# Kernel tuning notes

Hardware: AMD Instinct MI355X
Metric: run time of the kernel (lower is better)

## Reference

```python
import jax, jax.numpy as jnp
import numpy as np

G, N, E = 16, 512, 2048        # graphs, nodes/graph, edges/graph
CN, CE = 64, 64                # node / edge feature channels
K = 3                          # Laguerre polynomial order
RATIO = 0.5
KEEP = int(np.ceil(RATIO * N)) # 256 kept nodes per graph (static)
POWER_ITERS = 64               # power iteration approximating eigsh(k=1,'LM')


def setup_inputs() -> dict:
    key = jax.random.key(0)
    ks = jax.random.split(key, 10)
    x_n = jax.random.normal(ks[0], (G * N, CN), jnp.float32)
    x_e = jax.random.normal(ks[1], (G * E, CE), jnp.float32)
    # incidence endpoints per edge, local node ids, no self loops
    u = jax.random.randint(ks[2], (G, E), 0, N)
    v = (u + 1 + jax.random.randint(ks[3], (G, E), 0, N - 1)) % N
    # node-level conv graph (global ids within per-graph blocks): both directions
    offs = (jnp.arange(G) * N)[:, None]
    src_n = jnp.concatenate([(u + offs).reshape(-1), (v + offs).reshape(-1)])
    dst_n = jnp.concatenate([(v + offs).reshape(-1), (u + offs).reshape(-1)])
    edge_weight_n = jax.random.uniform(ks[4], (src_n.shape[0],), jnp.float32)
    # edge-level conv graph (global ids within per-graph edge blocks)
    ME = 4 * E
    offs_e = (jnp.arange(G) * E)[:, None]
    src_e = (jax.random.randint(ks[5], (G, ME), 0, E) + offs_e).reshape(-1)
    dst_e = (jax.random.randint(ks[6], (G, ME), 0, E) + offs_e).reshape(-1)
    edge_weight_e = jax.random.uniform(ks[7], (src_e.shape[0],), jnp.float32)
    # HodgeLaguerreConv(C -> 1, K) weights (glorot-ish) + bias (zeros init)
    W_n = jax.random.normal(ks[8], (K, CN), jnp.float32) / np.sqrt(CN)
    b_n = jnp.zeros((1,), jnp.float32)
    W_e = jax.random.normal(ks[9], (K, CE), jnp.float32) / np.sqrt(CE)
    b_e = jnp.zeros((1,), jnp.float32)
    return dict(x_n=x_n, x_e=x_e, edge_u=u, edge_v=v,
                src_n=src_n, dst_n=dst_n, edge_weight_n=edge_weight_n,
                src_e=src_e, dst_e=dst_e, edge_weight_e=edge_weight_e,
                W_n=W_n, b_n=b_n, W_e=W_e, b_e=b_e)


def hodge_laguerre(x, src, dst, w, Wk, b):
    """HodgeLaguerreConv with out_channels=1: out = sum_k T_k(L) x @ Wk[k] + b.
    T_0 = x; T_1 = x - Lx; T_{k+1} = (-L T_k + (2k+1) T_k - k T_{k-1})/(k+1)."""
    num = x.shape[0]
    def L(z):  # scatter-add message passing: out[i] = sum_{j->i} norm * z[j]
        return jax.ops.segment_sum(w[:, None] * z[src], dst, num_segments=num)
    Tx0 = x
    out = Tx0 @ Wk[0]
    Tx1 = x - L(x)
    out = out + Tx1 @ Wk[1]
    k = 1
    for i in range(2, Wk.shape[0]):
        Tx2 = (-L(Tx1) + (2 * k + 1) * Tx1 - k * Tx0) / (k + 1)
        out = out + Tx2 @ Wk[i]
        Tx0, Tx1 = Tx1, Tx2
        k += 1
    return out + b[0]


def pool_graph(sn, se, xn, xe, u, v):
    # node score augmented by |B1| @ edge_score (abs incidence gathers both endpoints)
    aug = sn.at[u].add(se).at[v].add(se)
    perm = jnp.argsort(-aug)                    # descending sort, take top KEEP
    mask_n = jnp.zeros((N,), xn.dtype).at[perm[:KEEP]].set(1.0)
    # mask_e = |B1|^T (1 - mask_n); keep edge iff both endpoints kept (== 0)
    bad = (1.0 - mask_n[u]) + (1.0 - mask_n[v])
    keep_e = (bad == 0.0).astype(xn.dtype)
    # dense incidence B1 [N, E]: -1 at source row, +1 at target row
    cols = jnp.arange(E)
    B = jnp.zeros((N, E), xn.dtype).at[u, cols].add(-1.0).at[v, cols].add(1.0)
    Bm = B * mask_n[:, None] * keep_e[None, :]  # row/col masking (zero-padded)
    L0 = Bm @ Bm.T                              # [N, N] node Laplacian
    L1 = Bm.T @ Bm                              # [E, E] edge Laplacian
    # power iteration for lambda_max(L0) (== eigsh k=1 'LM'; zero rows keep spectrum)
    w = jnp.ones((N,), xn.dtype) / np.sqrt(N)
    for _ in range(POWER_ITERS):
        w = L0 @ w
        w = w / (jnp.linalg.norm(w) + 1e-12)
    lam = w @ (L0 @ w)
    scale = 2.0 / (lam + 1e-12)
    return xn * mask_n[:, None], L0 * scale, xe * keep_e[:, None], L1 * scale


def reference(x_n, x_e, edge_u, edge_v, src_n, dst_n, edge_weight_n,
              src_e, dst_e, edge_weight_e, W_n, b_n, W_e, b_e):
    score_n = jax.nn.sigmoid(hodge_laguerre(x_n, src_n, dst_n, edge_weight_n, W_n, b_n).reshape(-1))
    score_e = jax.nn.sigmoid(hodge_laguerre(x_e, src_e, dst_e, edge_weight_e, W_e, b_e).reshape(-1))
    xn_g = (x_n * score_n[:, None]).reshape(G, N, CN)
    xe_g = (x_e * score_e[:, None]).reshape(G, E, CE)
    sn = score_n.reshape(G, N)
    se = score_e.reshape(G, E)
    return jax.vmap(pool_graph)(sn, se, xn_g, xe_g, edge_u, edge_v)
```

## Files before the change

kernel.cpp:

```cpp
#include <hip/hip_runtime.h>
#include <math.h>

#define GG 16
#define NNODE 512
#define EEDGE 2048
#define KEEPN 256
#define PITERS 64
#define NNT 8192
#define NET 32768

typedef float vfloat4 __attribute__((ext_vector_type(4)));

#define WS_C1N 0
#define WS_C2N 8192
#define WS_BN  16384
#define WS_C1E 24576
#define WS_C2E 57344
#define WS_BE  90112
#define WS_SNW 122880
#define WS_SEW 131072
#define WS_KLIST 163840
#define WS_KCNT 196608
#define WS_SCALE 196624

#define O_XN 0
#define O_L0 524288
#define O_XE 4718592
#define O_L1 6815744

#define L04 1048576
#define ZTOT4 17825792
#define ZA4 6291456

__global__ __launch_bounds__(256) void k_dots(const float* __restrict__ xn,
    const float* __restrict__ xe, const float* __restrict__ Wn,
    const float* __restrict__ We, float* __restrict__ ws, float* __restrict__ out) {
  if (blockIdx.x >= 10240) {
    vfloat4 z = (vfloat4)(0.f);
    vfloat4* o4 = (vfloat4*)out;
    int start = (blockIdx.x - 10240) * 256 + threadIdx.x;
    #pragma unroll
    for (int n = 0; n < 24; ++n) {
      int i = start + n * 262144;
      int f = (i < L04) ? (O_L0 / 4 + i) : (O_L1 / 4 + (i - L04));
      __builtin_nontemporal_store(z, &o4[f]);
    }
    return;
  }
  int gw = (blockIdx.x * 256 + threadIdx.x) >> 6;
  int lane = threadIdx.x & 63;
  const float* x; const float* W; int row; float *c1, *c2, *bs;
  if (gw < NNT) {
    row = gw; x = xn + (size_t)row * 64; W = Wn;
    c1 = ws + WS_C1N; c2 = ws + WS_C2N; bs = ws + WS_BN;
  } else {
    row = gw - NNT;
    x = xe + (size_t)row * 64; W = We;
    c1 = ws + WS_C1E; c2 = ws + WS_C2E; bs = ws + WS_BE;
  }
  float v = x[lane];
  float r0 = v * W[lane];
  float r1 = v * W[64 + lane];
  float r2 = v * W[128 + lane];
  for (int o = 32; o; o >>= 1) {
    r0 += __shfl_xor(r0, o, 64);
    r1 += __shfl_xor(r1, o, 64);
    r2 += __shfl_xor(r2, o, 64);
  }
  if (lane == 0) { c1[row] = r1; c2[row] = r2; bs[row] = r0 + r1 + r2; }
}

#define SM_AUG 0
#define SM_SNW 512
#define SM_RED 1024
#define SM_IWS 1032
#define SM_KCP 1040
#define SM_S0  1056
#define SM_TOT 9256
#define DCAP 12
__global__ __launch_bounds__(512) void k_pool(
    const int* __restrict__ src_n, const int* __restrict__ dst_n, const float* __restrict__ wn,
    const int* __restrict__ src_e, const int* __restrict__ dst_e, const float* __restrict__ we,
    const int* __restrict__ edge_u, const int* __restrict__ edge_v,
    const float* __restrict__ bnp, const float* __restrict__ bep,
    float* __restrict__ ws, float* __restrict__ out) {
  const int tid = threadIdx.x;
  if (blockIdx.x >= 16) {
    vfloat4 z = (vfloat4)(0.f);
    vfloat4* o4 = (vfloat4*)out;
    int start = ZA4 + (blockIdx.x - 16) * 512 + tid;
    #pragma unroll
    for (int n = 0; n < 11; ++n) {
      int i = start + n * 1048576;
      __builtin_nontemporal_store(z, &o4[O_L1 / 4 + (i - L04)]);
    }
    return;
  }
  __shared__ float smem[SM_TOT];
  int* smi = (int*)smem;
  float* aug = smem + SM_AUG;
  float* snw = smem + SM_SNW;
  float* red = smem + SM_RED;
  int*   iws = smi + SM_IWS;
  int*   kcp = smi + SM_KCP;

  const int g = blockIdx.x;
  const int roffN = g * NNODE;
  const int roffE = g * EEDGE;
  const int lane = tid & 63, wid = tid >> 6;
  float biasN = bnp[0], biasE = bep[0];

  {
    float* c1n = smem + SM_S0;
    float* c2n = smem + SM_S0 + 512;
    float* d1n = smem + SM_S0 + 1024;
    float* d2n = smem + SM_S0 + 1536;
    float* e2n = smem + SM_S0 + 2048;
    c1n[tid] = ws[WS_C1N + roffN + tid];
    c2n[tid] = ws[WS_C2N + roffN + tid];
    d1n[tid] = 0.f; d2n[tid] = 0.f; e2n[tid] = 0.f;
    __syncthreads();
    for (int t = tid; t < 4096; t += 512) {
      int idx = (t < 2048) ? (g * 2048 + t) : (32768 + g * 2048 + (t - 2048));
      int s = src_n[idx] - roffN, d = dst_n[idx] - roffN;
      float w = wn[idx];
      atomicAdd(&d1n[d], w * c1n[s]);
      atomicAdd(&d2n[d], w * c2n[s]);
    }
    __syncthreads();
    for (int t = tid; t < 4096; t += 512) {
      int idx = (t < 2048) ? (g * 2048 + t) : (32768 + g * 2048 + (t - 2048));
      int s = src_n[idx] - roffN, d = dst_n[idx] - roffN;
      atomicAdd(&e2n[d], wn[idx] * d2n[s]);
    }
    __syncthreads();
    float t = ws[WS_BN + roffN + tid] - d1n[tid] - 2.0f * d2n[tid]
            + 0.5f * e2n[tid] + biasN;
    float s = 1.0f / (1.0f + expf(-t));
    snw[tid] = s; aug[tid] = s;
    __syncthreads();
  }

  float* seS = smem + SM_S0 + 2048;
  int*   suv = smi + SM_S0;
  {
    float* c1e = smem + SM_S0;
    float* c2e = smem + SM_S0 + 2048;
    float* d1e = smem + SM_S0 + 4096;
    float* d2e = smem + SM_S0 + 6144;
    float* e2e = smem + SM_S0;
    for (int i = tid; i < EEDGE; i += 512) {
      c1e[i] = ws[WS_C1E + roffE + i];
      c2e[i] = ws[WS_C2E + roffE + i];
      d1e[i] = 0.f; d2e[i] = 0.f;
    }
    __syncthreads();
    for (int t = tid; t < 8192; t += 512) {
      int idx = g * 8192 + t;
      int s = src_e[idx] - roffE, d = dst_e[idx] - roffE;
      float w = we[idx];
      atomicAdd(&d1e[d], w * c1e[s]);
      atomicAdd(&d2e[d], w * c2e[s]);
    }
    __syncthreads();
    for (int i = tid; i < EEDGE; i += 512) e2e[i] = 0.f;
    __syncthreads();
    for (int t = tid; t < 8192; t += 512) {
      int idx = g * 8192 + t;
      int s = src_e[idx] - roffE, d = dst_e[idx] - roffE;
      atomicAdd(&e2e[d], we[idx] * d2e[s]);
    }
    __syncthreads();
    for (int e = tid; e < EEDGE; e += 512) {
      float t = ws[WS_BE + roffE + e] - d1e[e] - 2.0f * d2e[e]
              + 0.5f * e2e[e] + biasE;
      float s = 1.0f / (1.0f + expf(-t));
      int u = edge_u[roffE + e], v = edge_v[roffE + e];
      seS[e] = s;
      suv[e] = u | (v << 16);
      atomicAdd(&aug[u], s);
      atomicAdd(&aug[v], s);
    }
    __syncthreads();
  }

  unsigned short* adjU = (unsigned short*)(smem + SM_S0 + 4096);
  float* wvA = smem + SM_S0 + 6144;
  float* wvB = smem + SM_S0 + 6660;
  int* maskS = smi + SM_S0 + 7176;
  int* degS  = smi + SM_S0 + 7688;
  int* offS  = smi + SM_SNW;

  {
    float a = aug[tid];
    int r = 0;
    #pragma unroll 8
    for (int j = 0; j < NNODE; ++j) {
      float b = aug[j];
      r += (b > a) || (b == a && j < tid);
    }
    maskS[tid] = (r < KEEPN) ? 1 : 0;
    degS[tid] = 0;
  }
  if (tid == 0) *kcp = 0;
  __syncthreads();
  ws[WS_SNW + roffN + tid] = snw[tid] * (float)maskS[tid];

  int* wsi = (int*)ws;
  for (int e = tid; e < EEDGE; e += 512) {
    int p2 = suv[e];
    int u = p2 & 0xffff, v = p2 >> 16;
    int k = maskS[u] & maskS[v];
    ws[WS_SEW + roffE + e] = seS[e] * (float)k;
    if (k) {
      int p = atomicAdd(kcp, 1);
      wsi[WS_KLIST + roffE + p] = e;
      atomicAdd(&degS[u], 1);
      atomicAdd(&degS[v], 1);
    }
  }
  __syncthreads();
  if (tid == 0) wsi[WS_KCNT + g] = *kcp;

  int dv = degS[tid];
  int inc = dv;
  for (int o = 1; o < 64; o <<= 1) {
    int t = __shfl_up(inc, o, 64);
    if (lane >= o) inc += t;
  }
  if (lane == 63) iws[wid] = inc;
  __syncthreads();
  int base = 0;
  for (int k = 0; k < wid; ++k) base += iws[k];
  int myStart = base + inc - dv;
  offS[tid] = myStart;
  __syncthreads();

  for (int e = tid; e < EEDGE; e += 512) {
    int p2 = suv[e];
    int u = p2 & 0xffff, v = p2 >> 16;
    if (maskS[u] & maskS[v]) {
      int pu = atomicAdd(&offS[u], 1); adjU[pu] = (unsigned short)v;
      int pv = atomicAdd(&offS[v], 1); adjU[pv] = (unsigned short)u;
    }
  }
  __syncthreads();
  int myDeg = dv;
  int myEnd = myStart + myDeg;

  int nbr[DCAP];
  #pragma unroll
  for (int k = 0; k < DCAP; ++k)
    nbr[k] = (k < myDeg) ? (int)adjU[myStart + k] : NNODE;
  bool ovf = myDeg > DCAP;

  wvA[tid] = 0.04419417382415922f;
  if (tid == 0) { wvA[NNODE] = 0.f; wvB[NNODE] = 0.f; }
  __syncthreads();
  float* wcur = wvA; float* wnext = wvB;
  for (int it = 0; it < PITERS; ++it) {
    float acc = (float)myDeg * wcur[tid];
    #pragma unroll
    for (int k = 0; k < DCAP; ++k) acc -= wcur[nbr[k]];
    if (ovf) for (int p = myStart + DCAP; p < myEnd; ++p) acc -= wcur[(int)adjU[p]];
    if ((it & 7) == 7) {
      float sq = acc * acc;
      for (int o = 32; o; o >>= 1) sq += __shfl_xor(sq, o, 64);
      if (lane == 0) red[wid] = sq;
      __syncthreads();
      float tot = red[0] + red[1] + red[2] + red[3]
                + red[4] + red[5] + red[6] + red[7];
      wnext[tid] = acc * (1.0f / (sqrtf(tot) + 1e-12f));
    } else {
      wnext[tid] = acc;
    }
    __syncthreads();
    float* tmp = wcur; wcur = wnext; wnext = tmp;
  }
  {
    float wv_ = wcur[tid];
    float acc = (float)myDeg * wv_;
    #pragma unroll
    for (int k = 0; k < DCAP; ++k) acc -= wcur[nbr[k]];
    if (ovf) for (int p = myStart + DCAP; p < myEnd; ++p) acc -= wcur[(int)adjU[p]];
    float pr = wv_ * acc;
    for (int o = 32; o; o >>= 1) pr += __shfl_xor(pr, o, 64);
    if (lane == 0) red[wid] = pr;
    __syncthreads();
    if (tid == 0) {
      float lam = red[0] + red[1] + red[2] + red[3]
                + red[4] + red[5] + red[6] + red[7];
      ws[WS_SCALE + g] = 2.0f / (lam + 1e-12f);
    }
  }
}

__global__ __launch_bounds__(256) void k_out(
    const float* __restrict__ xn, const float* __restrict__ xe,
    const int* __restrict__ edge_u, const int* __restrict__ edge_v,
    const float* __restrict__ ws, float* __restrict__ out) {
  int b = blockIdx.x, tid = threadIdx.x;
  const int* wsi = (const int*)ws;
  if (b < 512) {
    int idx = b * 256 + tid;
    int row = idx >> 4;
    float s = ws[WS_SNW + row];
    float4 x4 = ((const float4*)xn)[idx];
    ((float4*)(out + O_XN))[idx] = make_float4(x4.x * s, x4.y * s, x4.z * s, x4.w * s);
  } else if (b < 2560) {
    int idx = (b - 512) * 256 + tid;
    int row = idx >> 4;
    float s = ws[WS_SEW + row];
    float4 x4 = ((const float4*)xe)[idx];
    ((float4*)(out + O_XE))[idx] = make_float4(x4.x * s, x4.y * s, x4.z * s, x4.w * s);
  } else if (b < 2576) {
    int g = b - 2560;
    int cnt = wsi[WS_KCNT + g];
    float s = ws[WS_SCALE + g];
    float* L0 = out + O_L0 + (long long)g * (NNODE * NNODE);
    const int* kl = wsi + WS_KLIST + g * EEDGE;
    const int* eu = edge_u + g * EEDGE;
    const int* ev = edge_v + g * EEDGE;
    for (int t = tid; t < cnt; t += 256) {
      int e = kl[t];
      int u = eu[e], v = ev[e];
      atomicAdd(&L0[u * NNODE + u], s);
      atomicAdd(&L0[v * NNODE + v], s);
      atomicAdd(&L0[u * NNODE + v], -s);
      atomicAdd(&L0[v * NNODE + u], -s);
    }
  } else {
    int q = b - 2576;
    int g = q >> 8, sb = q & 255;
    int cnt = wsi[WS_KCNT + g];
    float s = ws[WS_SCALE + g];
    float* L1 = out + O_L1 + (long long)g * (EEDGE * EEDGE);
    const int* kl = wsi + WS_KLIST + g * EEDGE;
    const int* eu = edge_u + g * EEDGE;
    const int* ev = edge_v + g * EEDGE;
    for (int a = sb; a < cnt; a += 256) {
      int e1 = kl[a];
      int u1 = eu[e1], v1 = ev[e1];
      long long rowoff = (long long)e1 * EEDGE;
      for (int b2 = tid; b2 < cnt; b2 += 256) {
        int e2 = kl[b2];
        int u2 = eu[e2], v2 = ev[e2];
        int val = (u1 == u2) + (v1 == v2) - (v1 == u2) - (u1 == v2);
        if (val) L1[rowoff + e2] = s * (float)val;
      }
    }
  }
}

extern "C" void kernel_launch(void* const* d_in, const int* in_sizes, int n_in,
                              void* d_out, int out_size, void* d_ws, size_t ws_size,
                              hipStream_t stream) {
  const float* x_n = (const float*)d_in[0];
  const float* x_e = (const float*)d_in[1];
  const int* edge_u = (const int*)d_in[2];
  const int* edge_v = (const int*)d_in[3];
  const int* src_n = (const int*)d_in[4];
  const int* dst_n = (const int*)d_in[5];
  const float* ew_n = (const float*)d_in[6];
  const int* src_e = (const int*)d_in[7];
  const int* dst_e = (const int*)d_in[8];
  const float* ew_e = (const float*)d_in[9];
  const float* W_n = (const float*)d_in[10];
  const float* b_n = (const float*)d_in[11];
  const float* W_e = (const float*)d_in[12];
  const float* b_e = (const float*)d_in[13];
  float* ws = (float*)d_ws;
  float* out = (float*)d_out;

  k_dots<<<10240 + 1024, 256, 0, stream>>>(x_n, x_e, W_n, W_e, ws, out);
  k_pool<<<16 + 2048, 512, 0, stream>>>(src_n, dst_n, ew_n, src_e, dst_e, ew_e,
                                        edge_u, edge_v, b_n, b_e, ws, out);
  k_out<<<6672, 256, 0, stream>>>(x_n, x_e, edge_u, edge_v, ws, out);
}
```

Before: 471.7 us.

## Fuse all three kernels into one cooperative persistent kernel with grid syncs

Replaces the three launches (dots, pool, output) with a single cooperative kernel of 256 blocks that uses grid-wide syncs between phases. The zeroing of the Laplacian outputs now runs in the 240 non-pool blocks while 16 blocks run the per-graph pooling. The aim is to remove launch gaps and overlap the large zero-fill with the serial pooling. In exchange, the dot phase, the final scaling and the L1 writes run on far fewer blocks, and a cooperative launch limits occupancy.

```diff
diff --git a/kernel.cpp b/kernel.cpp
--- a/kernel.cpp
+++ b/kernel.cpp
@@ -1,5 +1,8 @@
 #include <hip/hip_runtime.h>
+#include <hip/hip_cooperative_groups.h>
 #include <math.h>
+
+namespace cg = cooperative_groups;
 
 #define GG 16
 #define NNODE 512
@@ -30,45 +33,10 @@
 
 #define L04 1048576
 #define ZTOT4 17825792
-#define ZA4 6291456
-
-__global__ __launch_bounds__(256) void k_dots(const float* __restrict__ xn,
-    const float* __restrict__ xe, const float* __restrict__ Wn,
-    const float* __restrict__ We, float* __restrict__ ws, float* __restrict__ out) {
-  if (blockIdx.x >= 10240) {
-    vfloat4 z = (vfloat4)(0.f);
-    vfloat4* o4 = (vfloat4*)out;
-    int start = (blockIdx.x - 10240) * 256 + threadIdx.x;
-    #pragma unroll
-    for (int n = 0; n < 24; ++n) {
-      int i = start + n * 262144;
-      int f = (i < L04) ? (O_L0 / 4 + i) : (O_L1 / 4 + (i - L04));
-      __builtin_nontemporal_store(z, &o4[f]);
-    }
-    return;
-  }
-  int gw = (blockIdx.x * 256 + threadIdx.x) >> 6;
-  int lane = threadIdx.x & 63;
-  const float* x; const float* W; int row; float *c1, *c2, *bs;
-  if (gw < NNT) {
-    row = gw; x = xn + (size_t)row * 64; W = Wn;
-    c1 = ws + WS_C1N; c2 = ws + WS_C2N; bs = ws + WS_BN;
-  } else {
-    row = gw - NNT;
-    x = xe + (size_t)row * 64; W = We;
-    c1 = ws + WS_C1E; c2 = ws + WS_C2E; bs = ws + WS_BE;
-  }
-  float v = x[lane];
-  float r0 = v * W[lane];
-  float r1 = v * W[64 + lane];
-  float r2 = v * W[128 + lane];
-  for (int o = 32; o; o >>= 1) {
-    r0 += __shfl_xor(r0, o, 64);
-    r1 += __shfl_xor(r1, o, 64);
-    r2 += __shfl_xor(r2, o, 64);
-  }
-  if (lane == 0) { c1[row] = r1; c2[row] = r2; bs[row] = r0 + r1 + r2; }
-}
+
+#define NBLK 256
+#define NTHR 512
+#define ZBLK (NBLK - 16)
 
 #define SM_AUG 0
 #define SM_SNW 512
@@ -78,250 +46,285 @@
 #define SM_S0  1056
 #define SM_TOT 9256
 #define DCAP 12
-__global__ __launch_bounds__(512) void k_pool(
+
+__global__ __launch_bounds__(NTHR) void k_fused(
+    const float* __restrict__ xn, const float* __restrict__ xe,
+    const float* __restrict__ Wn, const float* __restrict__ We,
     const int* __restrict__ src_n, const int* __restrict__ dst_n, const float* __restrict__ wn,
     const int* __restrict__ src_e, const int* __restrict__ dst_e, const float* __restrict__ we,
     const int* __restrict__ edge_u, const int* __restrict__ edge_v,
     const float* __restrict__ bnp, const float* __restrict__ bep,
     float* __restrict__ ws, float* __restrict__ out) {
   const int tid = threadIdx.x;
-  if (blockIdx.x >= 16) {
+  const int bid = blockIdx.x;
+  __shared__ float smem[SM_TOT];
+  cg::grid_group grid = cg::this_grid();
+
+  {
+    const int lane = tid & 63;
+    const int gwave = (bid * NTHR + tid) >> 6;
+    #pragma unroll 2
+    for (int n = 0; n < 20; ++n) {
+      int gw = gwave + n * 2048;
+      const float* x; const float* W; int row; float *c1, *c2, *bs;
+      if (gw < NNT) {
+        row = gw; x = xn + (size_t)row * 64; W = Wn;
+        c1 = ws + WS_C1N; c2 = ws + WS_C2N; bs = ws + WS_BN;
+      } else {
+        row = gw - NNT;
+        x = xe + (size_t)row * 64; W = We;
+        c1 = ws + WS_C1E; c2 = ws + WS_C2E; bs = ws + WS_BE;
+      }
+      float v = x[lane];
+      float r0 = v * W[lane];
+      float r1 = v * W[64 + lane];
+      float r2 = v * W[128 + lane];
+      for (int o = 32; o; o >>= 1) {
+        r0 += __shfl_xor(r0, o, 64);
+        r1 += __shfl_xor(r1, o, 64);
+        r2 += __shfl_xor(r2, o, 64);
+      }
+      if (lane == 0) { c1[row] = r1; c2[row] = r2; bs[row] = r0 + r1 + r2; }
+    }
+  }
+  grid.sync();
+
+  if (bid >= 16) {
     vfloat4 z = (vfloat4)(0.f);
     vfloat4* o4 = (vfloat4*)out;
-    int start = ZA4 + (blockIdx.x - 16) * 512 + tid;
+    for (int i = (bid - 16) * NTHR + tid; i < ZTOT4; i += ZBLK * NTHR) {
+      int f = (i < L04) ? (O_L0 / 4 + i) : (O_L1 / 4 + (i - L04));
+      __builtin_nontemporal_store(z, &o4[f]);
+    }
+  } else {
+    int* smi = (int*)smem;
+    float* aug = smem + SM_AUG;
+    float* snw = smem + SM_SNW;
+    float* red = smem + SM_RED;
+    int*   iws = smi + SM_IWS;
+    int*   kcp = smi + SM_KCP;
+
+    const int g = bid;
+    const int roffN = g * NNODE;
+    const int roffE = g * EEDGE;
+    const int lane = tid & 63, wid = tid >> 6;
+    float biasN = bnp[0], biasE = bep[0];
+
+    {
+      float* c1n = smem + SM_S0;
+      float* c2n = smem + SM_S0 + 512;
+      float* d1n = smem + SM_S0 + 1024;
+      float* d2n = smem + SM_S0 + 1536;
+      float* e2n = smem + SM_S0 + 2048;
+      c1n[tid] = ws[WS_C1N + roffN + tid];
+      c2n[tid] = ws[WS_C2N + roffN + tid];
+      d1n[tid] = 0.f; d2n[tid] = 0.f; e2n[tid] = 0.f;
+      __syncthreads();
+      for (int t = tid; t < 4096; t += 512) {
+        int idx = (t < 2048) ? (g * 2048 + t) : (32768 + g * 2048 + (t - 2048));
+        int s = src_n[idx] - roffN, d = dst_n[idx] - roffN;
+        float w = wn[idx];
+        atomicAdd(&d1n[d], w * c1n[s]);
+        atomicAdd(&d2n[d], w * c2n[s]);
+      }
+      __syncthreads();
+      for (int t = tid; t < 4096; t += 512) {
+        int idx = (t < 2048) ? (g * 2048 + t) : (32768 + g * 2048 + (t - 2048));
+        int s = src_n[idx] - roffN, d = dst_n[idx] - roffN;
+        atomicAdd(&e2n[d], wn[idx] * d2n[s]);
+      }
+      __syncthreads();
+      float t = ws[WS_BN + roffN + tid] - d1n[tid] - 2.0f * d2n[tid]
+              + 0.5f * e2n[tid] + biasN;
+      float s = 1.0f / (1.0f + expf(-t));
+      snw[tid] = s; aug[tid] = s;
+      __syncthreads();
+    }
+
+    float* seS = smem + SM_S0 + 2048;
+    int*   suv = smi + SM_S0;
+    {
+      float* c1e = smem + SM_S0;
+      float* c2e = smem + SM_S0 + 2048;
+      float* d1e = smem + SM_S0 + 4096;
+      float* d2e = smem + SM_S0 + 6144;
+      float* e2e = smem + SM_S0;
+      for (int i = tid; i < EEDGE; i += 512) {
+        c1e[i] = ws[WS_C1E + roffE + i];
+        c2e[i] = ws[WS_C2E + roffE + i];
+        d1e[i] = 0.f; d2e[i] = 0.f;
+      }
+      __syncthreads();
+      for (int t = tid; t < 8192; t += 512) {
+        int idx = g * 8192 + t;
+        int s = src_e[idx] - roffE, d = dst_e[idx] - roffE;
+        float w = we[idx];
+        atomicAdd(&d1e[d], w * c1e[s]);
+        atomicAdd(&d2e[d], w * c2e[s]);
+      }
+      __syncthreads();
+      for (int i = tid; i < EEDGE; i += 512) e2e[i] = 0.f;
+      __syncthreads();
+      for (int t = tid; t < 8192; t += 512) {
+        int idx = g * 8192 + t;
+        int s = src_e[idx] - roffE, d = dst_e[idx] - roffE;
+        atomicAdd(&e2e[d], we[idx] * d2e[s]);
+      }
+      __syncthreads();
+      for (int e = tid; e < EEDGE; e += 512) {
+        float t = ws[WS_BE + roffE + e] - d1e[e] - 2.0f * d2e[e]
+                + 0.5f * e2e[e] + biasE;
+        float s = 1.0f / (1.0f + expf(-t));
+        int u = edge_u[roffE + e], v = edge_v[roffE + e];
+        seS[e] = s;
+        suv[e] = u | (v << 16);
+        atomicAdd(&aug[u], s);
+        atomicAdd(&aug[v], s);
+      }
+      __syncthreads();
+    }
+
+    unsigned short* adjU = (unsigned short*)(smem + SM_S0 + 4096);
+    float* wvA = smem + SM_S0 + 6144;
+    float* wvB = smem + SM_S0 + 6660;
+    int* maskS = smi + SM_S0 + 7176;
+    int* degS  = smi + SM_S0 + 7688;
+    int* offS  = smi + SM_SNW;
+
+    {
+      float a = aug[tid];
+      int r = 0;
+      #pragma unroll 8
+      for (int j = 0; j < NNODE; ++j) {
+        float b = aug[j];
+        r += (b > a) || (b == a && j < tid);
+      }
+      maskS[tid] = (r < KEEPN) ? 1 : 0;
+      degS[tid] = 0;
+    }
+    if (tid == 0) *kcp = 0;
+    __syncthreads();
+    ws[WS_SNW + roffN + tid] = snw[tid] * (float)maskS[tid];
+
+    int* wsi = (int*)ws;
+    for (int e = tid; e < EEDGE; e += 512) {
+      int p2 = suv[e];
+      int u = p2 & 0xffff, v = p2 >> 16;
+      int k = maskS[u] & maskS[v];
+      ws[WS_SEW + roffE + e] = seS[e] * (float)k;
+      if (k) {
+        int p = atomicAdd(kcp, 1);
+        wsi[WS_KLIST + roffE + p] = e;
+        atomicAdd(&degS[u], 1);
+        atomicAdd(&degS[v], 1);
+      }
+    }
+    __syncthreads();
+    if (tid == 0) wsi[WS_KCNT + g] = *kcp;
+
+    int dv = degS[tid];
+    int inc = dv;
+    for (int o = 1; o < 64; o <<= 1) {
+      int t = __shfl_up(inc, o, 64);
+      if (lane >= o) inc += t;
+    }
+    if (lane == 63) iws[wid] = inc;
+    __syncthreads();
+    int base = 0;
+    for (int k = 0; k < wid; ++k) base += iws[k];
+    int myStart = base + inc - dv;
+    offS[tid] = myStart;
+    __syncthreads();
+
+    for (int e = tid; e < EEDGE; e += 512) {
+      int p2 = suv[e];
+      int u = p2 & 0xffff, v = p2 >> 16;
+      if (maskS[u] & maskS[v]) {
+        int pu = atomicAdd(&offS[u], 1); adjU[pu] = (unsigned short)v;
+        int pv = atomicAdd(&offS[v], 1); adjU[pv] = (unsigned short)u;
+      }
+    }
+    __syncthreads();
+    int myDeg = dv;
+    int myEnd = myStart + myDeg;
+
+    int nbr[DCAP];
     #pragma unroll
-    for (int n = 0; n < 11; ++n) {
-      int i = start + n * 1048576;
-      __builtin_nontemporal_store(z, &o4[O_L1 / 4 + (i - L04)]);
-    }
-    return;
-  }
-  __shared__ float smem[SM_TOT];
-  int* smi = (int*)smem;
-  float* aug = smem + SM_AUG;
-  float* snw = smem + SM_SNW;
-  float* red = smem + SM_RED;
-  int*   iws = smi + SM_IWS;
-  int*   kcp = smi + SM_KCP;
-
-  const int g = blockIdx.x;
-  const int roffN = g * NNODE;
-  const int roffE = g * EEDGE;
-  const int lane = tid & 63, wid = tid >> 6;
-  float biasN = bnp[0], biasE = bep[0];
-
+    for (int k = 0; k < DCAP; ++k)
+      nbr[k] = (k < myDeg) ? (int)adjU[myStart + k] : NNODE;
+    bool ovf = myDeg > DCAP;
+
+    wvA[tid] = 0.04419417382415922f;
+    if (tid == 0) { wvA[NNODE] = 0.f; wvB[NNODE] = 0.f; }
+    __syncthreads();
+    float* wcur = wvA; float* wnext = wvB;
+    for (int it = 0; it < PITERS; ++it) {
+      float acc = (float)myDeg * wcur[tid];
+      #pragma unroll
+      for (int k = 0; k < DCAP; ++k) acc -= wcur[nbr[k]];
+      if (ovf) for (int p = myStart + DCAP; p < myEnd; ++p) acc -= wcur[(int)adjU[p]];
+      if ((it & 7) == 7) {
+        float sq = acc * acc;
+        for (int o = 32; o; o >>= 1) sq += __shfl_xor(sq, o, 64);
+        if (lane == 0) red[wid] = sq;
+        __syncthreads();
+        float tot = red[0] + red[1] + red[2] + red[3]
+                  + red[4] + red[5] + red[6] + red[7];
+        wnext[tid] = acc * (1.0f / (sqrtf(tot) + 1e-12f));
+      } else {
+        wnext[tid] = acc;
+      }
+      __syncthreads();
+      float* tmp = wcur; wcur = wnext; wnext = tmp;
+    }
+    {
+      float wv_ = wcur[tid];
+      float acc = (float)myDeg * wv_;
+      #pragma unroll
+      for (int k = 0; k < DCAP; ++k) acc -= wcur[nbr[k]];
+      if (ovf) for (int p = myStart + DCAP; p < myEnd; ++p) acc -= wcur[(int)adjU[p]];
+      float pr = wv_ * acc;
+      for (int o = 32; o; o >>= 1) pr += __shfl_xor(pr, o, 64);
+      if (lane == 0) red[wid] = pr;
+      __syncthreads();
+      if (tid == 0) {
+        float lam = red[0] + red[1] + red[2] + red[3]
+                  + red[4] + red[5] + red[6] + red[7];
+        ws[WS_SCALE + g] = 2.0f / (lam + 1e-12f);
+      }
+    }
+  }
+  grid.sync();
+
+  const int* wsi2 = (const int*)ws;
   {
-    float* c1n = smem + SM_S0;
-    float* c2n = smem + SM_S0 + 512;
-    float* d1n = smem + SM_S0 + 1024;
-    float* d2n = smem + SM_S0 + 1536;
-    float* e2n = smem + SM_S0 + 2048;
-    c1n[tid] = ws[WS_C1N + roffN + tid];
-    c2n[tid] = ws[WS_C2N + roffN + tid];
-    d1n[tid] = 0.f; d2n[tid] = 0.f; e2n[tid] = 0.f;
-    __syncthreads();
-    for (int t = tid; t < 4096; t += 512) {
-      int idx = (t < 2048) ? (g * 2048 + t) : (32768 + g * 2048 + (t - 2048));
-      int s = src_n[idx] - roffN, d = dst_n[idx] - roffN;
-      float w = wn[idx];
-      atomicAdd(&d1n[d], w * c1n[s]);
-      atomicAdd(&d2n[d], w * c2n[s]);
-    }
-    __syncthreads();
-    for (int t = tid; t < 4096; t += 512) {
-      int idx = (t < 2048) ? (g * 2048 + t) : (32768 + g * 2048 + (t - 2048));
-      int s = src_n[idx] - roffN, d = dst_n[idx] - roffN;
-      atomicAdd(&e2n[d], wn[idx] * d2n[s]);
-    }
-    __syncthreads();
-    float t = ws[WS_BN + roffN + tid] - d1n[tid] - 2.0f * d2n[tid]
-            + 0.5f * e2n[tid] + biasN;
-    float s = 1.0f / (1.0f + expf(-t));
-    snw[tid] = s; aug[tid] = s;
-    __syncthreads();
-  }
-
-  float* seS = smem + SM_S0 + 2048;
-  int*   suv = smi + SM_S0;
-  {
-    float* c1e = smem + SM_S0;
-    float* c2e = smem + SM_S0 + 2048;
-    float* d1e = smem + SM_S0 + 4096;
-    float* d2e = smem + SM_S0 + 6144;
-    float* e2e = smem + SM_S0;
-    for (int i = tid; i < EEDGE; i += 512) {
-      c1e[i] = ws[WS_C1E + roffE + i];
-      c2e[i] = ws[WS_C2E + roffE + i];
-      d1e[i] = 0.f; d2e[i] = 0.f;
-    }
-    __syncthreads();
-    for (int t = tid; t < 8192; t += 512) {
-      int idx = g * 8192 + t;
-      int s = src_e[idx] - roffE, d = dst_e[idx] - roffE;
-      float w = we[idx];
-      atomicAdd(&d1e[d], w * c1e[s]);
-      atomicAdd(&d2e[d], w * c2e[s]);
-    }
-    __syncthreads();
-    for (int i = tid; i < EEDGE; i += 512) e2e[i] = 0.f;
-    __syncthreads();
-    for (int t = tid; t < 8192; t += 512) {
-      int idx = g * 8192 + t;
-      int s = src_e[idx] - roffE, d = dst_e[idx] - roffE;
-      atomicAdd(&e2e[d], we[idx] * d2e[s]);
-    }
-    __syncthreads();
-    for (int e = tid; e < EEDGE; e += 512) {
-      float t = ws[WS_BE + roffE + e] - d1e[e] - 2.0f * d2e[e]
-              + 0.5f * e2e[e] + biasE;
-      float s = 1.0f / (1.0f + expf(-t));
-      int u = edge_u[roffE + e], v = edge_v[roffE + e];
-      seS[e] = s;
-      suv[e] = u | (v << 16);
-      atomicAdd(&aug[u], s);
-      atomicAdd(&aug[v], s);
-    }
-    __syncthreads();
-  }
-
-  unsigned short* adjU = (unsigned short*)(smem + SM_S0 + 4096);
-  float* wvA = smem + SM_S0 + 6144;
-  float* wvB = smem + SM_S0 + 6660;
-  int* maskS = smi + SM_S0 + 7176;
-  int* degS  = smi + SM_S0 + 7688;
-  int* offS  = smi + SM_SNW;
-
-  {
-    float a = aug[tid];
-    int r = 0;
-    #pragma unroll 8
-    for (int j = 0; j < NNODE; ++j) {
-      float b = aug[j];
-      r += (b > a) || (b == a && j < tid);
-    }
-    maskS[tid] = (r < KEEPN) ? 1 : 0;
-    degS[tid] = 0;
-  }
-  if (tid == 0) *kcp = 0;
-  __syncthreads();
-  ws[WS_SNW + roffN + tid] = snw[tid] * (float)maskS[tid];
-
-  int* wsi = (int*)ws;
-  for (int e = tid; e < EEDGE; e += 512) {
-    int p2 = suv[e];
-    int u = p2 & 0xffff, v = p2 >> 16;
-    int k = maskS[u] & maskS[v];
-    ws[WS_SEW + roffE + e] = seS[e] * (float)k;
-    if (k) {
-      int p = atomicAdd(kcp, 1);
-      wsi[WS_KLIST + roffE + p] = e;
-      atomicAdd(&degS[u], 1);
-      atomicAdd(&degS[v], 1);
-    }
-  }
-  __syncthreads();
-  if (tid == 0) wsi[WS_KCNT + g] = *kcp;
-
-  int dv = degS[tid];
-  int inc = dv;
-  for (int o = 1; o < 64; o <<= 1) {
-    int t = __shfl_up(inc, o, 64);
-    if (lane >= o) inc += t;
-  }
-  if (lane == 63) iws[wid] = inc;
-  __syncthreads();
-  int base = 0;
-  for (int k = 0; k < wid; ++k) base += iws[k];
-  int myStart = base + inc - dv;
-  offS[tid] = myStart;
-  __syncthreads();
-
-  for (int e = tid; e < EEDGE; e += 512) {
-    int p2 = suv[e];
-    int u = p2 & 0xffff, v = p2 >> 16;
-    if (maskS[u] & maskS[v]) {
-      int pu = atomicAdd(&offS[u], 1); adjU[pu] = (unsigned short)v;
-      int pv = atomicAdd(&offS[v], 1); adjU[pv] = (unsigned short)u;
-    }
-  }
-  __syncthreads();
-  int myDeg = dv;
-  int myEnd = myStart + myDeg;
-
-  int nbr[DCAP];
-  #pragma unroll
-  for (int k = 0; k < DCAP; ++k)
-    nbr[k] = (k < myDeg) ? (int)adjU[myStart + k] : NNODE;
-  bool ovf = myDeg > DCAP;
-
-  wvA[tid] = 0.04419417382415922f;
-  if (tid == 0) { wvA[NNODE] = 0.f; wvB[NNODE] = 0.f; }
-  __syncthreads();
-  float* wcur = wvA; float* wnext = wvB;
-  for (int it = 0; it < PITERS; ++it) {
-    float acc = (float)myDeg * wcur[tid];
+    int u = bid * NTHR + tid;
     #pragma unroll
-    for (int k = 0; k < DCAP; ++k) acc -= wcur[nbr[k]];
-    if (ovf) for (int p = myStart + DCAP; p < myEnd; ++p) acc -= wcur[(int)adjU[p]];
-    if ((it & 7) == 7) {
-      float sq = acc * acc;
-      for (int o = 32; o; o >>= 1) sq += __shfl_xor(sq, o, 64);
-      if (lane == 0) red[wid] = sq;
-      __syncthreads();
-      float tot = red[0] + red[1] + red[2] + red[3]
-                + red[4] + red[5] + red[6] + red[7];
-      wnext[tid] = acc * (1.0f / (sqrtf(tot) + 1e-12f));
-    } else {
-      wnext[tid] = acc;
-    }
-    __syncthreads();
-    float* tmp = wcur; wcur = wnext; wnext = tmp;
-  }
-  {
-    float wv_ = wcur[tid];
-    float acc = (float)myDeg * wv_;
-    #pragma unroll
-    for (int k = 0; k < DCAP; ++k) acc -= wcur[nbr[k]];
-    if (ovf) for (int p = myStart + DCAP; p < myEnd; ++p) acc -= wcur[(int)adjU[p]];
-    float pr = wv_ * acc;
-    for (int o = 32; o; o >>= 1) pr += __shfl_xor(pr, o, 64);
-    if (lane == 0) red[wid] = pr;
-    __syncthreads();
-    if (tid == 0) {
-      float lam = red[0] + red[1] + red[2] + red[3]
-                + red[4] + red[5] + red[6] + red[7];
-      ws[WS_SCALE + g] = 2.0f / (lam + 1e-12f);
-    }
-  }
-}
-
-__global__ __launch_bounds__(256) void k_out(
-    const float* __restrict__ xn, const float* __restrict__ xe,
-    const int* __restrict__ edge_u, const int* __restrict__ edge_v,
-    const float* __restrict__ ws, float* __restrict__ out) {
-  int b = blockIdx.x, tid = threadIdx.x;
-  const int* wsi = (const int*)ws;
-  if (b < 512) {
-    int idx = b * 256 + tid;
-    int row = idx >> 4;
-    float s = ws[WS_SNW + row];
-    float4 x4 = ((const float4*)xn)[idx];
-    ((float4*)(out + O_XN))[idx] = make_float4(x4.x * s, x4.y * s, x4.z * s, x4.w * s);
-  } else if (b < 2560) {
-    int idx = (b - 512) * 256 + tid;
-    int row = idx >> 4;
-    float s = ws[WS_SEW + row];
-    float4 x4 = ((const float4*)xe)[idx];
-    ((float4*)(out + O_XE))[idx] = make_float4(x4.x * s, x4.y * s, x4.z * s, x4.w * s);
-  } else if (b < 2576) {
-    int g = b - 2560;
-    int cnt = wsi[WS_KCNT + g];
+    for (int k = 0; k < 5; ++k) {
+      if (u < 131072) {
+        int row = u >> 4;
+        float s = ws[WS_SNW + row];
+        float4 x4 = ((const float4*)xn)[u];
+        ((float4*)(out + O_XN))[u] = make_float4(x4.x * s, x4.y * s, x4.z * s, x4.w * s);
+      } else {
+        int idx = u - 131072;
+        int row = idx >> 4;
+        float s = ws[WS_SEW + row];
+        float4 x4 = ((const float4*)xe)[idx];
+        ((float4*)(out + O_XE))[idx] = make_float4(x4.x * s, x4.y * s, x4.z * s, x4.w * s);
+      }
+      u += NBLK * NTHR;
+    }
+  }
+  if (bid >= 16 && bid < 32) {
+    int g = bid - 16;
+    int cnt = wsi2[WS_KCNT + g];
     float s = ws[WS_SCALE + g];
     float* L0 = out + O_L0 + (long long)g * (NNODE * NNODE);
-    const int* kl = wsi + WS_KLIST + g * EEDGE;
+    const int* kl = wsi2 + WS_KLIST + g * EEDGE;
     const int* eu = edge_u + g * EEDGE;
     const int* ev = edge_v + g * EEDGE;
-    for (int t = tid; t < cnt; t += 256) {
+    for (int t = tid; t < cnt; t += NTHR) {
       int e = kl[t];
       int u = eu[e], v = ev[e];
       atomicAdd(&L0[u * NNODE + u], s);
@@ -329,20 +332,21 @@
       atomicAdd(&L0[u * NNODE + v], -s);
       atomicAdd(&L0[v * NNODE + u], -s);
     }
-  } else {
-    int q = b - 2576;
+  }
+  for (int it = 0; it < 16; ++it) {
+    int q = bid * 16 + it;
     int g = q >> 8, sb = q & 255;
-    int cnt = wsi[WS_KCNT + g];
+    int cnt = wsi2[WS_KCNT + g];
     float s = ws[WS_SCALE + g];
     float* L1 = out + O_L1 + (long long)g * (EEDGE * EEDGE);
-    const int* kl = wsi + WS_KLIST + g * EEDGE;
+    const int* kl = wsi2 + WS_KLIST + g * EEDGE;
     const int* eu = edge_u + g * EEDGE;
     const int* ev = edge_v + g * EEDGE;
     for (int a = sb; a < cnt; a += 256) {
       int e1 = kl[a];
       int u1 = eu[e1], v1 = ev[e1];
       long long rowoff = (long long)e1 * EEDGE;
-      for (int b2 = tid; b2 < cnt; b2 += 256) {
+      for (int b2 = tid; b2 < cnt; b2 += NTHR) {
         int e2 = kl[b2];
         int u2 = eu[e2], v2 = ev[e2];
         int val = (u1 == u2) + (v1 == v2) - (v1 == u2) - (u1 == v2);
@@ -372,8 +376,13 @@
   float* ws = (float*)d_ws;
   float* out = (float*)d_out;
 
-  k_dots<<<10240 + 1024, 256, 0, stream>>>(x_n, x_e, W_n, W_e, ws, out);
-  k_pool<<<16 + 2048, 512, 0, stream>>>(src_n, dst_n, ew_n, src_e, dst_e, ew_e,
-                                        edge_u, edge_v, b_n, b_e, ws, out);
-  k_out<<<6672, 256, 0, stream>>>(x_n, x_e, edge_u, edge_v, ws, out);
+  void* args[] = {
+    (void*)&x_n, (void*)&x_e, (void*)&W_n, (void*)&W_e,
+    (void*)&src_n, (void*)&dst_n, (void*)&ew_n,
+    (void*)&src_e, (void*)&dst_e, (void*)&ew_e,
+    (void*)&edge_u, (void*)&edge_v, (void*)&b_n, (void*)&b_e,
+    (void*)&ws, (void*)&out
+  };
+  hipLaunchCooperativeKernel((const void*)k_fused, dim3(NBLK), dim3(NTHR),
+                             args, 0, stream);
 }
```

Result: slower. 555.7 us (+17.8%).

## Split pool kernel into graph and power stages and spread output zero-fill

Applied to the files above, without the earlier changes.

The per-graph pooling kernel is split into two kernels. k_graph builds the mask and adjacency and writes degree, start offsets and adjacency to the workspace. k_power reloads them and runs the power iteration. The zeroing of the large L0/L1 output is divided across three launches so that the few 16-block serial stages run alongside bulk stores, and the dot-product kernel now handles five rows per wave with 512-thread blocks. This adds a launch and a workspace round trip for the adjacency, and reuses workspace regions that must not collide with live data.

```diff
diff --git a/kernel.cpp b/kernel.cpp
--- a/kernel.cpp
+++ b/kernel.cpp
@@ -23,6 +23,10 @@
 #define WS_KCNT 196608
 #define WS_SCALE 196624
 
+#define WS_DEG_I   0
+#define WS_START_I 8192
+#define WS_ADJ_I   24576
+
 #define O_XN 0
 #define O_L0 524288
 #define O_XE 4718592
@@ -30,44 +34,53 @@
 
 #define L04 1048576
 #define ZTOT4 17825792
-#define ZA4 6291456
-
-__global__ __launch_bounds__(256) void k_dots(const float* __restrict__ xn,
-    const float* __restrict__ xe, const float* __restrict__ Wn,
-    const float* __restrict__ We, float* __restrict__ ws, float* __restrict__ out) {
-  if (blockIdx.x >= 10240) {
+#define ZB_LO 6291456
+#define ZC_LO 12582912
+
+#define DCAP 12
+
+__global__ __launch_bounds__(512) void k_front(
+    const float* __restrict__ xn, const float* __restrict__ xe,
+    const float* __restrict__ Wn, const float* __restrict__ We,
+    float* __restrict__ ws, float* __restrict__ out) {
+  const int tid = threadIdx.x, bid = blockIdx.x;
+  if (bid >= 1024) {
     vfloat4 z = (vfloat4)(0.f);
     vfloat4* o4 = (vfloat4*)out;
-    int start = (blockIdx.x - 10240) * 256 + threadIdx.x;
+    int base = (bid - 1024) * 512 + tid;
     #pragma unroll
-    for (int n = 0; n < 24; ++n) {
-      int i = start + n * 262144;
+    for (int n = 0; n < 12; ++n) {
+      int i = base + n * 524288;
       int f = (i < L04) ? (O_L0 / 4 + i) : (O_L1 / 4 + (i - L04));
       __builtin_nontemporal_store(z, &o4[f]);
     }
     return;
   }
-  int gw = (blockIdx.x * 256 + threadIdx.x) >> 6;
-  int lane = threadIdx.x & 63;
-  const float* x; const float* W; int row; float *c1, *c2, *bs;
-  if (gw < NNT) {
-    row = gw; x = xn + (size_t)row * 64; W = Wn;
-    c1 = ws + WS_C1N; c2 = ws + WS_C2N; bs = ws + WS_BN;
-  } else {
-    row = gw - NNT;
-    x = xe + (size_t)row * 64; W = We;
-    c1 = ws + WS_C1E; c2 = ws + WS_C2E; bs = ws + WS_BE;
-  }
-  float v = x[lane];
-  float r0 = v * W[lane];
-  float r1 = v * W[64 + lane];
-  float r2 = v * W[128 + lane];
-  for (int o = 32; o; o >>= 1) {
-    r0 += __shfl_xor(r0, o, 64);
-    r1 += __shfl_xor(r1, o, 64);
-    r2 += __shfl_xor(r2, o, 64);
-  }
-  if (lane == 0) { c1[row] = r1; c2[row] = r2; bs[row] = r0 + r1 + r2; }
+  const int lane = tid & 63;
+  const int wv = (bid * 512 + tid) >> 6;
+  #pragma unroll
+  for (int n = 0; n < 5; ++n) {
+    int gw = wv + n * 8192;
+    const float* x; const float* W; int row; float *c1, *c2, *bs;
+    if (gw < NNT) {
+      row = gw; x = xn + (size_t)row * 64; W = Wn;
+      c1 = ws + WS_C1N; c2 = ws + WS_C2N; bs = ws + WS_BN;
+    } else {
+      row = gw - NNT;
+      x = xe + (size_t)row * 64; W = We;
+      c1 = ws + WS_C1E; c2 = ws + WS_C2E; bs = ws + WS_BE;
+    }
+    float v = x[lane];
+    float r0 = v * W[lane];
+    float r1 = v * W[64 + lane];
+    float r2 = v * W[128 + lane];
+    for (int o = 32; o; o >>= 1) {
+      r0 += __shfl_xor(r0, o, 64);
+      r1 += __shfl_xor(r1, o, 64);
+      r2 += __shfl_xor(r2, o, 64);
+    }
+    if (lane == 0) { c1[row] = r1; c2[row] = r2; bs[row] = r0 + r1 + r2; }
+  }
 }
 
 #define SM_AUG 0
@@ -77,8 +90,7 @@
 #define SM_KCP 1040
 #define SM_S0  1056
 #define SM_TOT 9256
-#define DCAP 12
-__global__ __launch_bounds__(512) void k_pool(
+__global__ __launch_bounds__(512) void k_graph(
     const int* __restrict__ src_n, const int* __restrict__ dst_n, const float* __restrict__ wn,
     const int* __restrict__ src_e, const int* __restrict__ dst_e, const float* __restrict__ we,
     const int* __restrict__ edge_u, const int* __restrict__ edge_v,
@@ -88,10 +100,10 @@
   if (blockIdx.x >= 16) {
     vfloat4 z = (vfloat4)(0.f);
     vfloat4* o4 = (vfloat4*)out;
-    int start = ZA4 + (blockIdx.x - 16) * 512 + tid;
+    int base = ZB_LO + (blockIdx.x - 16) * 512 + tid;
     #pragma unroll
-    for (int n = 0; n < 11; ++n) {
-      int i = start + n * 1048576;
+    for (int n = 0; n < 12; ++n) {
+      int i = base + n * 524288;
       __builtin_nontemporal_store(z, &o4[O_L1 / 4 + (i - L04)]);
     }
     return;
@@ -100,7 +112,6 @@
   int* smi = (int*)smem;
   float* aug = smem + SM_AUG;
   float* snw = smem + SM_SNW;
-  float* red = smem + SM_RED;
   int*   iws = smi + SM_IWS;
   int*   kcp = smi + SM_KCP;
 
@@ -185,8 +196,6 @@
   }
 
   unsigned short* adjU = (unsigned short*)(smem + SM_S0 + 4096);
-  float* wvA = smem + SM_S0 + 6144;
-  float* wvB = smem + SM_S0 + 6660;
   int* maskS = smi + SM_S0 + 7176;
   int* degS  = smi + SM_S0 + 7688;
   int* offS  = smi + SM_SNW;
@@ -245,8 +254,52 @@
     }
   }
   __syncthreads();
-  int myDeg = dv;
+
+  wsi[WS_DEG_I + roffN + tid] = dv;
+  wsi[WS_START_I + roffN + tid] = myStart;
+  {
+    int* adjI = (int*)adjU;
+    for (int i = tid; i < 2048; i += 512)
+      wsi[WS_ADJ_I + roffE + i] = adjI[i];
+  }
+}
+
+#define PSM_ADJ 0
+#define PSM_WVA 2048
+#define PSM_WVB 2564
+#define PSM_RED 3080
+#define PSM_TOT 3088
+__global__ __launch_bounds__(512) void k_power(
+    float* __restrict__ ws, float* __restrict__ out) {
+  const int tid = threadIdx.x;
+  if (blockIdx.x >= 16) {
+    vfloat4 z = (vfloat4)(0.f);
+    vfloat4* o4 = (vfloat4*)out;
+    int base = ZC_LO + (blockIdx.x - 16) * 512 + tid;
+    #pragma unroll
+    for (int n = 0; n < 10; ++n) {
+      int i = base + n * 524288;
+      __builtin_nontemporal_store(z, &o4[O_L1 / 4 + (i - L04)]);
+    }
+    return;
+  }
+  __shared__ float smem[PSM_TOT];
+  int* smi = (int*)smem;
+  unsigned short* adjU = (unsigned short*)(smi + PSM_ADJ);
+  float* wvA = smem + PSM_WVA;
+  float* wvB = smem + PSM_WVB;
+  float* red = smem + PSM_RED;
+
+  const int g = blockIdx.x;
+  const int lane = tid & 63, wid = tid >> 6;
+  const int* wsi = (const int*)ws;
+
+  for (int i = tid; i < 2048; i += 512)
+    smi[PSM_ADJ + i] = wsi[WS_ADJ_I + g * EEDGE + i];
+  int myDeg = wsi[WS_DEG_I + g * NNODE + tid];
+  int myStart = wsi[WS_START_I + g * NNODE + tid];
   int myEnd = myStart + myDeg;
+  __syncthreads();
 
   int nbr[DCAP];
   #pragma unroll
@@ -372,8 +425,9 @@
   float* ws = (float*)d_ws;
   float* out = (float*)d_out;
 
-  k_dots<<<10240 + 1024, 256, 0, stream>>>(x_n, x_e, W_n, W_e, ws, out);
-  k_pool<<<16 + 2048, 512, 0, stream>>>(src_n, dst_n, ew_n, src_e, dst_e, ew_e,
-                                        edge_u, edge_v, b_n, b_e, ws, out);
+  k_front<<<2048, 512, 0, stream>>>(x_n, x_e, W_n, W_e, ws, out);
+  k_graph<<<16 + 1024, 512, 0, stream>>>(src_n, dst_n, ew_n, src_e, dst_e, ew_e,
+                                         edge_u, edge_v, b_n, b_e, ws, out);
+  k_power<<<16 + 1024, 512, 0, stream>>>(ws, out);
   k_out<<<6672, 256, 0, stream>>>(x_n, x_e, edge_u, edge_v, ws, out);
 }
```

Result: faster. 459.8 us (-2.5%).

## Move all output zero-fill into front kernel and loop dot-product waves

Applied to the files above, without the earlier changes.

Merges the output zeroing that was split between the dot kernel and the pool kernel into a single front kernel with 512-thread blocks. Each wave there now handles five rows of dot products. The 16-block pool kernel loses its extra zero-fill blocks and becomes a pure per-graph pipeline. The aim is to stop the serial pool stage from sharing the GPU with heavy store traffic, at the cost of a longer front kernel.

```diff
diff --git a/kernel.cpp b/kernel.cpp
--- a/kernel.cpp
+++ b/kernel.cpp
@@ -30,44 +30,51 @@
 
 #define L04 1048576
 #define ZTOT4 17825792
-#define ZA4 6291456
-
-__global__ __launch_bounds__(256) void k_dots(const float* __restrict__ xn,
-    const float* __restrict__ xe, const float* __restrict__ Wn,
-    const float* __restrict__ We, float* __restrict__ ws, float* __restrict__ out) {
-  if (blockIdx.x >= 10240) {
+
+#define DCAP 12
+
+__global__ __launch_bounds__(512) void k_front(
+    const float* __restrict__ xn, const float* __restrict__ xe,
+    const float* __restrict__ Wn, const float* __restrict__ We,
+    float* __restrict__ ws, float* __restrict__ out) {
+  const int tid = threadIdx.x, bid = blockIdx.x;
+  if (bid >= 1024) {
     vfloat4 z = (vfloat4)(0.f);
     vfloat4* o4 = (vfloat4*)out;
-    int start = (blockIdx.x - 10240) * 256 + threadIdx.x;
+    int base = (bid - 1024) * 512 + tid;
     #pragma unroll
-    for (int n = 0; n < 24; ++n) {
-      int i = start + n * 262144;
+    for (int n = 0; n < 17; ++n) {
+      int i = base + n * 1048576;
       int f = (i < L04) ? (O_L0 / 4 + i) : (O_L1 / 4 + (i - L04));
       __builtin_nontemporal_store(z, &o4[f]);
     }
     return;
   }
-  int gw = (blockIdx.x * 256 + threadIdx.x) >> 6;
-  int lane = threadIdx.x & 63;
-  const float* x; const float* W; int row; float *c1, *c2, *bs;
-  if (gw < NNT) {
-    row = gw; x = xn + (size_t)row * 64; W = Wn;
-    c1 = ws + WS_C1N; c2 = ws + WS_C2N; bs = ws + WS_BN;
-  } else {
-    row = gw - NNT;
-    x = xe + (size_t)row * 64; W = We;
-    c1 = ws + WS_C1E; c2 = ws + WS_C2E; bs = ws + WS_BE;
-  }
-  float v = x[lane];
-  float r0 = v * W[lane];
-  float r1 = v * W[64 + lane];
-  float r2 = v * W[128 + lane];
-  for (int o = 32; o; o >>= 1) {
-    r0 += __shfl_xor(r0, o, 64);
-    r1 += __shfl_xor(r1, o, 64);
-    r2 += __shfl_xor(r2, o, 64);
-  }
-  if (lane == 0) { c1[row] = r1; c2[row] = r2; bs[row] = r0 + r1 + r2; }
+  const int lane = tid & 63;
+  const int wv = (bid * 512 + tid) >> 6;
+  #pragma unroll
+  for (int n = 0; n < 5; ++n) {
+    int gw = wv + n * 8192;
+    const float* x; const float* W; int row; float *c1, *c2, *bs;
+    if (gw < NNT) {
+      row = gw; x = xn + (size_t)row * 64; W = Wn;
+      c1 = ws + WS_C1N; c2 = ws + WS_C2N; bs = ws + WS_BN;
+    } else {
+      row = gw - NNT;
+      x = xe + (size_t)row * 64; W = We;
+      c1 = ws + WS_C1E; c2 = ws + WS_C2E; bs = ws + WS_BE;
+    }
+    float v = x[lane];
+    float r0 = v * W[lane];
+    float r1 = v * W[64 + lane];
+    float r2 = v * W[128 + lane];
+    for (int o = 32; o; o >>= 1) {
+      r0 += __shfl_xor(r0, o, 64);
+      r1 += __shfl_xor(r1, o, 64);
+      r2 += __shfl_xor(r2, o, 64);
+    }
+    if (lane == 0) { c1[row] = r1; c2[row] = r2; bs[row] = r0 + r1 + r2; }
+  }
 }
 
 #define SM_AUG 0
@@ -77,25 +84,13 @@
 #define SM_KCP 1040
 #define SM_S0  1056
 #define SM_TOT 9256
-#define DCAP 12
-__global__ __launch_bounds__(512) void k_pool(
+__global__ __launch_bounds__(512) void k_pipe(
     const int* __restrict__ src_n, const int* __restrict__ dst_n, const float* __restrict__ wn,
     const int* __restrict__ src_e, const int* __restrict__ dst_e, const float* __restrict__ we,
     const int* __restrict__ edge_u, const int* __restrict__ edge_v,
     const float* __restrict__ bnp, const float* __restrict__ bep,
-    float* __restrict__ ws, float* __restrict__ out) {
+    float* __restrict__ ws) {
   const int tid = threadIdx.x;
-  if (blockIdx.x >= 16) {
-    vfloat4 z = (vfloat4)(0.f);
-    vfloat4* o4 = (vfloat4*)out;
-    int start = ZA4 + (blockIdx.x - 16) * 512 + tid;
-    #pragma unroll
-    for (int n = 0; n < 11; ++n) {
-      int i = start + n * 1048576;
-      __builtin_nontemporal_store(z, &o4[O_L1 / 4 + (i - L04)]);
-    }
-    return;
-  }
   __shared__ float smem[SM_TOT];
   int* smi = (int*)smem;
   float* aug = smem + SM_AUG;
@@ -372,8 +367,8 @@
   float* ws = (float*)d_ws;
   float* out = (float*)d_out;
 
-  k_dots<<<10240 + 1024, 256, 0, stream>>>(x_n, x_e, W_n, W_e, ws, out);
-  k_pool<<<16 + 2048, 512, 0, stream>>>(src_n, dst_n, ew_n, src_e, dst_e, ew_e,
-                                        edge_u, edge_v, b_n, b_e, ws, out);
+  k_front<<<3072, 512, 0, stream>>>(x_n, x_e, W_n, W_e, ws, out);
+  k_pipe<<<16, 512, 0, stream>>>(src_n, dst_n, ew_n, src_e, dst_e, ew_e,
+                                 edge_u, edge_v, b_n, b_e, ws);
   k_out<<<6672, 256, 0, stream>>>(x_n, x_e, edge_u, edge_v, ws, out);
 }
```

Result: slower. 489.0 us (+3.7%).
